# Kernel optimization log

Measured on AMD Instinct MI355X. Metric: run time of the kernel, lower is better.

Reference implementation:

```python
import jax, jax.numpy as jnp
import numpy as np

B, NSEQ, SEQ_PER = 2, 4, 256
S = NSEQ * SEQ_PER            # total sequence (stocks interleaved along seq dim)
D, H, HD = 1024, 16, 64       # d_model, nhead, head_dim
HD2, HD4 = HD // 2, HD // 4
DFF = 4096
LAMBDA_INIT = 0.2             # lambda_init_fn(0) = 0.8 - 0.6*exp(0)
SCALING = 1.0 / float(np.sqrt(HD2))
EPS_DEF = float(np.finfo(np.float32).eps)   # torch RMSNorm default eps (eps=None)
EPS_ATTN = 1e-5


def _rms(x, w, eps):
    return x * jax.lax.rsqrt(jnp.mean(x * x, axis=-1, keepdims=True) + eps) * w


def _rope(x, fc):
    # x: (B, T, NSEQ, 2H, HD2); fc: (T, HD4, 2) holding (cos, sin)
    xr = x.reshape(x.shape[:-1] + (HD4, 2))
    c = fc[None, :, None, None, :, 0]
    s = fc[None, :, None, None, :, 1]
    x0, x1 = xr[..., 0], xr[..., 1]
    return jnp.stack([x0 * c - x1 * s, x0 * s + x1 * c], axis=-1).reshape(x.shape)


def setup_inputs():
    key = jax.random.key(0)
    ks = jax.random.split(key, 16)
    def w(i, shape, std=0.02):
        return jax.random.normal(ks[i], shape, jnp.float32) * std
    # true RoPE table for seq_per_stock-1 positions
    t = jnp.arange(SEQ_PER - 1, dtype=jnp.float32)[:, None]
    inv = 1.0 / (10000.0 ** (jnp.arange(HD4, dtype=jnp.float32) / HD4))
    ang = t * inv[None, :]
    return {
        "x": jax.random.normal(ks[0], (B, S, D), jnp.float32),
        "freqs_cis": jnp.stack([jnp.cos(ang), jnp.sin(ang)], axis=-1),
        "w_norm1": jnp.ones((D,), jnp.float32),
        "w_norm2": jnp.ones((D,), jnp.float32),
        "Wq": w(1, (H * HD, D)), "bq": jnp.zeros((H * HD,), jnp.float32),
        "Wk": w(2, (H * HD, D)), "bk": jnp.zeros((H * HD,), jnp.float32),
        "Wv": w(3, (H * HD, D)), "bv": jnp.zeros((H * HD,), jnp.float32),
        "Wo": w(4, (D, H * HD)), "bo": jnp.zeros((D,), jnp.float32),
        "lq1": w(5, (HD2,), 0.1), "lk1": w(6, (HD2,), 0.1),
        "lq2": w(7, (HD2,), 0.1), "lk2": w(8, (HD2,), 0.1),
        "w_attn_norm": jnp.ones((HD,), jnp.float32),
        "Wg": w(9, (2 * DFF, D)), "bg": jnp.zeros((2 * DFF,), jnp.float32),
        "Wout": w(10, (D, DFF)), "bout": jnp.zeros((D,), jnp.float32),
    }


def reference(x, freqs_cis, w_norm1, w_norm2, Wq, bq, Wk, bk, Wv, bv, Wo, bo,
              lq1, lk1, lq2, lk2, w_attn_norm, Wg, bg, Wout, bout):
    Bz, Sz, _ = x.shape
    h = _rms(x, w_norm1, EPS_DEF)
    q = (h @ Wq.T + bq).reshape(Bz, SEQ_PER, NSEQ, 2 * H, HD2)
    k = (h @ Wk.T + bk).reshape(Bz, SEQ_PER, NSEQ, 2 * H, HD2)
    v = (h @ Wv.T + bv).reshape(Bz, Sz, H, HD).transpose(0, 2, 1, 3)   # (B,H,S,HD), interleaved order
    # RoPE on all but the first per-stock timestep; same freqs for every stock
    q = jnp.concatenate([q[:, :1], _rope(q[:, 1:], freqs_cis)], axis=1)
    k = jnp.concatenate([k[:, :1], _rope(k[:, 1:], freqs_cis)], axis=1)
    # reorder q/k to stock-major flat sequence (torch permute(0,4,1,2,3)+reshape)
    q = q.transpose(0, 2, 1, 3, 4).reshape(Bz, Sz, 2 * H, HD2).transpose(0, 2, 1, 3)
    k = k.transpose(0, 2, 1, 3, 4).reshape(Bz, Sz, 2 * H, HD2).transpose(0, 2, 1, 3)
    scores = jnp.einsum('bhqd,bhkd->bhqk', q, k) * SCALING              # (B,2H,S,S)
    causal = jnp.triu(jnp.ones((SEQ_PER, SEQ_PER), bool), 1)
    mask = jnp.tile(causal, (NSEQ, NSEQ))   # block-tiled causal, as torch .repeat
    att = jnp.sign(scores) * jax.nn.softmax(
        jnp.where(mask, -1e30, jnp.abs(scores)), axis=-1)
    lam = jnp.exp(jnp.sum(lk1 * lq1)) - jnp.exp(jnp.sum(lk2 * lq2)) + LAMBDA_INIT
    att = att.reshape(Bz, H, 2, Sz, Sz)
    a1, a2 = att[:, :, 0], att[:, :, 1]
    G = jnp.mean(a1, axis=-2, keepdims=True)          # mean over queries, broadcast back
    a = jnp.where(mask, 0.0, a1 - lam * a2 + lam * G)
    ao = jnp.einsum('bhqk,bhkd->bhqd', a, v)          # v kept in interleaved order (faithful to source)
    ao = _rms(ao, w_attn_norm, EPS_ATTN)
    ao = ao.reshape(Bz, Sz, H * HD)  # flat reinterpret (B,H,S,HD)->(B,S,H*HD), matches torch reshape chain
    x = x + ao @ Wo.T + bo
    h2 = _rms(x, w_norm2, EPS_DEF)
    u, vg = jnp.split(h2 @ Wg.T + bg, 2, axis=-1)
    return x + (u * jax.nn.silu(vg)) @ Wout.T + bout
```

## Files before the change

### kernel.cpp

```cpp
#include <hip/hip_runtime.h>

#define LAMBDA_INIT 0.2f
#define SCALING 0.17677669529663687f
#define EPS_DEF 1.1920928955078125e-07f
#define EPS_ATTN 1e-5f

typedef unsigned short us4 __attribute__((ext_vector_type(4)));
typedef unsigned short us8v __attribute__((ext_vector_type(8)));
typedef float f32x4 __attribute__((ext_vector_type(4)));
typedef float f32x2 __attribute__((ext_vector_type(2)));
typedef __bf16 bf16x8 __attribute__((ext_vector_type(8)));

#define MFMA16(a, b, c) __builtin_amdgcn_mfma_f32_16x16x32_bf16((a), (b), (c), 0, 0, 0)

__device__ __forceinline__ float bf2f(unsigned short u) {
    unsigned int x = ((unsigned int)u) << 16;
    return __builtin_bit_cast(float, x);
}
__device__ __forceinline__ unsigned short f2bf(float f) {
    unsigned int x = __builtin_bit_cast(unsigned int, f);
    x += 0x7fffu + ((x >> 16) & 1u);
    return (unsigned short)(x >> 16);
}
__device__ __forceinline__ void split8(f32x4 a, f32x4 b, us8v& hi, us8v& lo) {
#pragma unroll
    for (int u = 0; u < 4; u++) {
        unsigned short h = f2bf(a[u]);
        hi[u] = h; lo[u] = f2bf(a[u] - bf2f(h));
        unsigned short h2 = f2bf(b[u]);
        hi[4 + u] = h2; lo[4 + u] = f2bf(b[u] - bf2f(h2));
    }
}
__device__ __forceinline__ bf16x8 ldb(const unsigned short* p) {
    return __builtin_bit_cast(bf16x8, *(const us8v*)p);
}

__device__ __forceinline__ float wave_sum(float v) {
#pragma unroll
    for (int o = 32; o > 0; o >>= 1) v += __shfl_down(v, o);
    return v;
}
__device__ __forceinline__ float block_sum(float v, float* red4) {
    int wv = threadIdx.x >> 6;
    float w = wave_sum(v);
    __syncthreads();
    if ((threadIdx.x & 63) == 0) red4[wv] = w;
    __syncthreads();
    return red4[0] + red4[1] + red4[2] + red4[3];
}

__global__ __launch_bounds__(256) void prep(float* __restrict__ G, float* __restrict__ lamp,
                                            const float* lq1, const float* lk1,
                                            const float* lq2, const float* lk2) {
    int i = (blockIdx.x * 256 + threadIdx.x) * 4;
    G[i] = 0.f; G[i + 1] = 0.f; G[i + 2] = 0.f; G[i + 3] = 0.f;
    if (blockIdx.x == 0 && threadIdx.x == 0) {
        float a = 0.f, c = 0.f;
        for (int d = 0; d < 32; d++) {
            a += lq1[d] * lk1[d];
            c += lq2[d] * lk2[d];
        }
        *lamp = expf(a) - expf(c) + LAMBDA_INIT;
    }
}

__global__ __launch_bounds__(256) void cvt_bf16(const float* __restrict__ s,
                                                unsigned short* __restrict__ d, int n4) {
    int i = blockIdx.x * 256 + threadIdx.x;
    if (i >= n4) return;
    f32x4 v = ((const f32x4*)s)[i];
    us4 o;
#pragma unroll
    for (int u = 0; u < 4; u++) o[u] = f2bf(v[u]);
    ((us4*)d)[i] = o;
}

__global__ __launch_bounds__(256) void cvt_split(const float* __restrict__ s,
                                                 unsigned short* __restrict__ hi,
                                                 unsigned short* __restrict__ lo, int n4) {
    int i = blockIdx.x * 256 + threadIdx.x;
    if (i >= n4) return;
    f32x4 v = ((const f32x4*)s)[i];
    us4 h, l;
#pragma unroll
    for (int u = 0; u < 4; u++) {
        h[u] = f2bf(v[u]);
        l[u] = f2bf(v[u] - bf2f(h[u]));
    }
    ((us4*)hi)[i] = h;
    ((us4*)lo)[i] = l;
}

template <int OUTBF>
__global__ __launch_bounds__(256) void rms_kernel(const float* __restrict__ x,
                                                  const float* __restrict__ w,
                                                  void* __restrict__ out, float eps) {
    int row = blockIdx.x;
    int tid = threadIdx.x;
    size_t base = (size_t)row * 1024 + tid * 4;
    f32x4 v = *(const f32x4*)(x + base);
    float ss = v[0]*v[0] + v[1]*v[1] + v[2]*v[2] + v[3]*v[3];
    __shared__ float red4[4];
    float tot = block_sum(ss, red4);
    float r = rsqrtf(tot * (1.0f / 1024.f) + eps);
    f32x4 wv = *(const f32x4*)(w + tid * 4);
    if (OUTBF) {
        us4 o;
#pragma unroll
        for (int i = 0; i < 4; i++) o[i] = f2bf(v[i] * r * wv[i]);
        *(us4*)((unsigned short*)out + base) = o;
    } else {
        f32x4 o;
#pragma unroll
        for (int i = 0; i < 4; i++) o[i] = v[i] * r * wv[i];
        *(f32x4*)((float*)out + base) = o;
    }
}

__global__ __launch_bounds__(256) void rms_split(const float* __restrict__ x,
                                                 const float* __restrict__ w,
                                                 unsigned short* __restrict__ hh,
                                                 unsigned short* __restrict__ hl, float eps) {
    int row = blockIdx.x;
    int tid = threadIdx.x;
    size_t base = (size_t)row * 1024 + tid * 4;
    f32x4 v = *(const f32x4*)(x + base);
    float ss = v[0]*v[0] + v[1]*v[1] + v[2]*v[2] + v[3]*v[3];
    __shared__ float red4[4];
    float tot = block_sum(ss, red4);
    float r = rsqrtf(tot * (1.0f / 1024.f) + eps);
    f32x4 wv = *(const f32x4*)(w + tid * 4);
    us4 oh, ol;
#pragma unroll
    for (int i = 0; i < 4; i++) {
        float val = v[i] * r * wv[i];
        oh[i] = f2bf(val);
        ol[i] = f2bf(val - bf2f(oh[i]));
    }
    *(us4*)(hh + base) = oh;
    *(us4*)(hl + base) = ol;
}

__global__ __launch_bounds__(256) void gemm_qkv_ps(
        const unsigned short* __restrict__ AH, const unsigned short* __restrict__ AL,
        const unsigned short* __restrict__ WqH, const unsigned short* __restrict__ WqL,
        const unsigned short* __restrict__ WkH, const unsigned short* __restrict__ WkL,
        const unsigned short* __restrict__ WvH, const unsigned short* __restrict__ WvL,
        const float* __restrict__ bq, const float* __restrict__ bk, const float* __restrict__ bv,
        float* __restrict__ Yq, float* __restrict__ Yk, float* __restrict__ Yv) {
    const int z = blockIdx.z;
    const unsigned short* BH = (z == 0) ? WqH : (z == 1) ? WkH : WvH;
    const unsigned short* BL = (z == 0) ? WqL : (z == 1) ? WkL : WvL;
    const float* bias = (z == 0) ? bq : (z == 1) ? bk : bv;
    float* out        = (z == 0) ? Yq : (z == 1) ? Yk : Yv;
    const int K = 1024, N = 1024;
    __shared__ __align__(16) unsigned short Ah[64][72];
    __shared__ __align__(16) unsigned short Al[64][72];
    __shared__ __align__(16) unsigned short Bh[64][72];
    __shared__ __align__(16) unsigned short Bl[64][72];
    const int t = threadIdx.x;
    const int bm = blockIdx.x, bn = blockIdx.y;
    const int lane = t & 63, w = t >> 6;
    const int wr = w >> 1, wc = w & 1;
    const int l15 = lane & 15, lg = lane >> 4;
    const int sr = t >> 2, sc = (t & 3) * 16;

    const unsigned short* AgH = AH + (size_t)(bm * 64 + sr) * K + sc;
    const unsigned short* AgL = AL + (size_t)(bm * 64 + sr) * K + sc;
    const unsigned short* BgH = BH + (size_t)(bn * 64 + sr) * K + sc;
    const unsigned short* BgL = BL + (size_t)(bn * 64 + sr) * K + sc;

    f32x4 acc[2][2] = {};

    for (int k0 = 0; k0 < K; k0 += 64) {
        us8v ah0 = *(const us8v*)(AgH + k0), ah1 = *(const us8v*)(AgH + k0 + 8);
        us8v al0 = *(const us8v*)(AgL + k0), al1 = *(const us8v*)(AgL + k0 + 8);
        us8v bh0 = *(const us8v*)(BgH + k0), bh1 = *(const us8v*)(BgH + k0 + 8);
        us8v bl0 = *(const us8v*)(BgL + k0), bl1 = *(const us8v*)(BgL + k0 + 8);
        __syncthreads();
        *(us8v*)&Ah[sr][sc] = ah0; *(us8v*)&Ah[sr][sc + 8] = ah1;
        *(us8v*)&Al[sr][sc] = al0; *(us8v*)&Al[sr][sc + 8] = al1;
        *(us8v*)&Bh[sr][sc] = bh0; *(us8v*)&Bh[sr][sc + 8] = bh1;
        *(us8v*)&Bl[sr][sc] = bl0; *(us8v*)&Bl[sr][sc + 8] = bl1;
        __syncthreads();
#pragma unroll
        for (int kk = 0; kk < 2; kk++) {
            bf16x8 afh[2], afl[2], bfh[2], bfl[2];
#pragma unroll
            for (int mi = 0; mi < 2; mi++) {
                afh[mi] = ldb(&Ah[wr * 32 + mi * 16 + l15][kk * 32 + lg * 8]);
                afl[mi] = ldb(&Al[wr * 32 + mi * 16 + l15][kk * 32 + lg * 8]);
            }
#pragma unroll
            for (int ni = 0; ni < 2; ni++) {
                bfh[ni] = ldb(&Bh[wc * 32 + ni * 16 + l15][kk * 32 + lg * 8]);
                bfl[ni] = ldb(&Bl[wc * 32 + ni * 16 + l15][kk * 32 + lg * 8]);
            }
#pragma unroll
            for (int mi = 0; mi < 2; mi++)
#pragma unroll
                for (int ni = 0; ni < 2; ni++) {
                    acc[mi][ni] = MFMA16(afl[mi], bfh[ni], acc[mi][ni]);
                    acc[mi][ni] = MFMA16(afh[mi], bfl[ni], acc[mi][ni]);
                    acc[mi][ni] = MFMA16(afh[mi], bfh[ni], acc[mi][ni]);
                }
        }
    }

    const int rbase = bm * 64 + wr * 32 + (lg << 2);
    const int cbase = bn * 64 + wc * 32 + l15;
#pragma unroll
    for (int mi = 0; mi < 2; mi++) {
#pragma unroll
        for (int ni = 0; ni < 2; ni++) {
            int col = cbase + ni * 16;
            float bb = bias[col];
#pragma unroll
            for (int r = 0; r < 4; r++) {
                int row = rbase + mi * 16 + r;
                out[(size_t)row * N + col] = acc[mi][ni][r] + bb;
            }
        }
    }
}

__global__ __launch_bounds__(256) void gemm_mfma_wb(const unsigned short* __restrict__ A,
                                                    const unsigned short* __restrict__ Bt,
                                                    const float* __restrict__ bias,
                                                    const float* __restrict__ res,
                                                    float* __restrict__ out,
                                                    int M, int N, int K) {
    __shared__ __align__(16) unsigned short As[64][72];
    __shared__ __align__(16) unsigned short Bs[64][72];
    const int t = threadIdx.x;
    const int bm = blockIdx.x, bn = blockIdx.y;
    const int lane = t & 63, w = t >> 6;
    const int wr = w >> 1, wc = w & 1;
    const int l15 = lane & 15, lg = lane >> 4;
    const int sr = t >> 2, sc = (t & 3) * 16;

    const unsigned short* Ag = A + (size_t)(bm * 64 + sr) * K + sc;
    const unsigned short* Bg = Bt + (size_t)(bn * 64 + sr) * K + sc;

    f32x4 acc[2][2] = {};

    for (int k0 = 0; k0 < K; k0 += 64) {
        us8v a0 = *(const us8v*)(Ag + k0);
        us8v a1 = *(const us8v*)(Ag + k0 + 8);
        us8v b0 = *(const us8v*)(Bg + k0);
        us8v b1 = *(const us8v*)(Bg + k0 + 8);
        __syncthreads();
        *(us8v*)&As[sr][sc]     = a0;
        *(us8v*)&As[sr][sc + 8] = a1;
        *(us8v*)&Bs[sr][sc]     = b0;
        *(us8v*)&Bs[sr][sc + 8] = b1;
        __syncthreads();
#pragma unroll
        for (int kk = 0; kk < 2; kk++) {
            bf16x8 af[2], bf[2];
#pragma unroll
            for (int mi = 0; mi < 2; mi++)
                af[mi] = ldb(&As[wr * 32 + mi * 16 + l15][kk * 32 + lg * 8]);
#pragma unroll
            for (int ni = 0; ni < 2; ni++)
                bf[ni] = ldb(&Bs[wc * 32 + ni * 16 + l15][kk * 32 + lg * 8]);
#pragma unroll
            for (int mi = 0; mi < 2; mi++)
#pragma unroll
                for (int ni = 0; ni < 2; ni++)
                    acc[mi][ni] = MFMA16(af[mi], bf[ni], acc[mi][ni]);
        }
    }

    const int rbase = bm * 64 + wr * 32 + (lg << 2);
    const int cbase = bn * 64 + wc * 32 + l15;
#pragma unroll
    for (int mi = 0; mi < 2; mi++) {
#pragma unroll
        for (int ni = 0; ni < 2; ni++) {
            int col = cbase + ni * 16;
            float bb = bias[col];
#pragma unroll
            for (int r = 0; r < 4; r++) {
                int row = rbase + mi * 16 + r;
                size_t oi = (size_t)row * N + col;
                out[oi] = acc[mi][ni][r] + bb + res[oi];
            }
        }
    }
}

__global__ __launch_bounds__(256) void gemm_gate_mfma(const unsigned short* __restrict__ A,
                                                      const float* __restrict__ Wg,
                                                      const float* __restrict__ bg,
                                                      unsigned short* __restrict__ mlp) {
    __shared__ __align__(16) unsigned short As[128][72];
    __shared__ __align__(16) unsigned short BsU[64][72];
    __shared__ __align__(16) unsigned short BsV[64][72];
    const int t = threadIdx.x;
    const int bm = blockIdx.x, bn = blockIdx.y;
    const int lane = t & 63, w = t >> 6;
    const int wr = w >> 1, wc = w & 1;
    const int l15 = lane & 15, lg = lane >> 4;
    const int sr = t >> 2, sc = (t & 3) * 16;

    const unsigned short* Ag  = A + (size_t)(bm * 128 + sr) * 1024 + sc;
    const unsigned short* Ag2 = Ag + (size_t)64 * 1024;
    const float* BgU = Wg + (size_t)(bn * 64 + sr) * 1024 + sc;
    const float* BgV = Wg + (size_t)(4096 + bn * 64 + sr) * 1024 + sc;

    f32x4 accU[4][2] = {};
    f32x4 accV[4][2] = {};

    for (int k0 = 0; k0 < 1024; k0 += 64) {
        us8v a0 = *(const us8v*)(Ag + k0);
        us8v a1 = *(const us8v*)(Ag + k0 + 8);
        us8v a2 = *(const us8v*)(Ag2 + k0);
        us8v a3 = *(const us8v*)(Ag2 + k0 + 8);
        f32x4 u0 = *(const f32x4*)(BgU + k0);
        f32x4 u1 = *(const f32x4*)(BgU + k0 + 4);
        f32x4 u2 = *(const f32x4*)(BgU + k0 + 8);
        f32x4 u3 = *(const f32x4*)(BgU + k0 + 12);
        f32x4 v0 = *(const f32x4*)(BgV + k0);
        f32x4 v1 = *(const f32x4*)(BgV + k0 + 4);
        f32x4 v2 = *(const f32x4*)(BgV + k0 + 8);
        f32x4 v3 = *(const f32x4*)(BgV + k0 + 12);
        us8v uw0, uw1, vw0, vw1;
#pragma unroll
        for (int u = 0; u < 4; u++) {
            uw0[u] = f2bf(u0[u]); uw0[4 + u] = f2bf(u1[u]);
            uw1[u] = f2bf(u2[u]); uw1[4 + u] = f2bf(u3[u]);
            vw0[u] = f2bf(v0[u]); vw0[4 + u] = f2bf(v1[u]);
            vw1[u] = f2bf(v2[u]); vw1[4 + u] = f2bf(v3[u]);
        }
        __syncthreads();
        *(us8v*)&As[sr][sc]          = a0;
        *(us8v*)&As[sr][sc + 8]      = a1;
        *(us8v*)&As[sr + 64][sc]     = a2;
        *(us8v*)&As[sr + 64][sc + 8] = a3;
        *(us8v*)&BsU[sr][sc]         = uw0;
        *(us8v*)&BsU[sr][sc + 8]     = uw1;
        *(us8v*)&BsV[sr][sc]         = vw0;
        *(us8v*)&BsV[sr][sc + 8]     = vw1;
        __syncthreads();
#pragma unroll
        for (int kk = 0; kk < 2; kk++) {
            bf16x8 af[4], bu[2], bv2[2];
#pragma unroll
            for (int mi = 0; mi < 4; mi++)
                af[mi] = ldb(&As[wr * 64 + mi * 16 + l15][kk * 32 + lg * 8]);
#pragma unroll
            for (int ni = 0; ni < 2; ni++) {
                bu[ni]  = ldb(&BsU[wc * 32 + ni * 16 + l15][kk * 32 + lg * 8]);
                bv2[ni] = ldb(&BsV[wc * 32 + ni * 16 + l15][kk * 32 + lg * 8]);
            }
#pragma unroll
            for (int mi = 0; mi < 4; mi++)
#pragma unroll
                for (int ni = 0; ni < 2; ni++) {
                    accU[mi][ni] = MFMA16(af[mi], bu[ni], accU[mi][ni]);
                    accV[mi][ni] = MFMA16(af[mi], bv2[ni], accV[mi][ni]);
                }
        }
    }

    const int rbase = bm * 128 + wr * 64 + (lg << 2);
    const int cbase = bn * 64 + wc * 32 + l15;
#pragma unroll
    for (int mi = 0; mi < 4; mi++) {
#pragma unroll
        for (int ni = 0; ni < 2; ni++) {
            int col = cbase + ni * 16;
            float bu_ = bg[col], bv_ = bg[4096 + col];
#pragma unroll
            for (int r = 0; r < 4; r++) {
                int row = rbase + mi * 16 + r;
                float u = accU[mi][ni][r] + bu_;
                float v = accV[mi][ni][r] + bv_;
                float s = v / (1.f + __expf(-v));
                mlp[(size_t)row * 4096 + col] = f2bf(u * s);
            }
        }
    }
}

__global__ __launch_bounds__(256) void rope_inplace(float* __restrict__ Y,
                                                    const float* __restrict__ fc) {
    int t = blockIdx.x;
    int s = t & 1023;
    int p = s >> 2;
    if (p == 0) return;
    int c0 = threadIdx.x * 4;
    float* y = Y + (size_t)t * 1024 + c0;
    int d4 = (c0 & 31) >> 1;
    f32x4 f = *(const f32x4*)(fc + ((size_t)(p - 1) * 16 + d4) * 2);
    float v0 = y[0], v1 = y[1], v2 = y[2], v3 = y[3];
    y[0] = v0 * f[0] - v1 * f[1];
    y[1] = v0 * f[1] + v1 * f[0];
    y[2] = v2 * f[2] - v3 * f[3];
    y[3] = v2 * f[3] + v3 * f[2];
}

__global__ __launch_bounds__(256) void rope_split_k(const float* __restrict__ Yk,
                                                    const float* __restrict__ fc,
                                                    unsigned short* __restrict__ KhG,
                                                    unsigned short* __restrict__ KlG) {
    int t = blockIdx.x;
    int s = t & 1023;
    int p = s >> 2;
    int c0 = threadIdx.x * 4;
    const float* y = Yk + (size_t)t * 1024 + c0;
    float v0 = y[0], v1 = y[1], v2 = y[2], v3 = y[3];
    if (p > 0) {
        int d4 = (c0 & 31) >> 1;
        f32x4 f = *(const f32x4*)(fc + ((size_t)(p - 1) * 16 + d4) * 2);
        float w0 = v0 * f[0] - v1 * f[1];
        float w1 = v0 * f[1] + v1 * f[0];
        float w2 = v2 * f[2] - v3 * f[3];
        float w3 = v2 * f[3] + v3 * f[2];
        v0 = w0; v1 = w1; v2 = w2; v3 = w3;
    }
    us4 hi, lo;
    hi[0] = f2bf(v0); lo[0] = f2bf(v0 - bf2f(hi[0]));
    hi[1] = f2bf(v1); lo[1] = f2bf(v1 - bf2f(hi[1]));
    hi[2] = f2bf(v2); lo[2] = f2bf(v2 - bf2f(hi[2]));
    hi[3] = f2bf(v3); lo[3] = f2bf(v3 - bf2f(hi[3]));
    *(us4*)(KhG + (size_t)t * 1024 + c0) = hi;
    *(us4*)(KlG + (size_t)t * 1024 + c0) = lo;
}

__global__ __launch_bounds__(256) void v_split_t(const float* __restrict__ Yv,
                                                 unsigned short* __restrict__ VtH,
                                                 unsigned short* __restrict__ VtL) {
    const int jc = blockIdx.x, h = blockIdx.y, b = blockIdx.z;
    __shared__ float tile[64][65];
    const int t = threadIdx.x;
    {
        const int jr = t >> 2, dc = (t & 3) * 16;
        const float* src = Yv + ((size_t)(b * 1024 + jc * 64 + jr) << 10) + h * 64 + dc;
        *(f32x4*)&tile[jr][dc]      = *(const f32x4*)src;
        *(f32x4*)&tile[jr][dc + 4]  = *(const f32x4*)(src + 4);
        *(f32x4*)&tile[jr][dc + 8]  = *(const f32x4*)(src + 8);
        *(f32x4*)&tile[jr][dc + 12] = *(const f32x4*)(src + 12);
    }
    __syncthreads();
    const int d = t >> 2, js = (t & 3) * 16;
    us8v h0, h1, l0, l1;
#pragma unroll
    for (int n = 0; n < 16; n++) {
        float val = tile[js + n][d];
        unsigned short hh = f2bf(val);
        unsigned short ll = f2bf(val - bf2f(hh));
        if (n < 8) { h0[n] = hh; l0[n] = ll; }
        else       { h1[n - 8] = hh; l1[n - 8] = ll; }
    }
    size_t ob = (((size_t)(b * 16 + h) * 64 + d) << 10) + jc * 64 + js;
    *(us8v*)(VtH + ob) = h0; *(us8v*)(VtH + ob + 8) = h1;
    *(us8v*)(VtL + ob) = l0; *(us8v*)(VtL + ob + 8) = l1;
}

__global__ __launch_bounds__(256) void pass_1(const float* __restrict__ Yq,
                                              const unsigned short* __restrict__ KhG,
                                              const unsigned short* __restrict__ KlG,
                                              const unsigned short* __restrict__ VtH,
                                              const unsigned short* __restrict__ VtL,
                                              const float* __restrict__ lamp,
                                              float* __restrict__ G,
                                              float* __restrict__ AOp) {
    const int blk = blockIdx.x;
    const int p  = blk >> 5;
    const int h  = blk & 15;
    const int b  = (blk >> 4) & 1;
    const int t = threadIdx.x;
    const int lane = t & 63, w = t >> 6;
    const int l15 = lane & 15, lg = lane >> 4;

    __shared__ __align__(16) unsigned short Kh[64][72];
    __shared__ __align__(16) unsigned short Kl[64][72];
    __shared__ __align__(16) unsigned short Vth[64][72];
    __shared__ __align__(16) unsigned short Vtl[64][72];
    __shared__ __align__(16) unsigned short Wh[64][72];
    __shared__ __align__(16) unsigned short Wl[64][72];
    __shared__ float Gacc[1024];

    for (int i = t; i < 1024; i += 256) Gacc[i] = 0.f;

    const int srow = t >> 2, ssub = t & 3;
    const int ptk = 4 * (srow & 15) + (srow >> 4);
    const unsigned short* KhB = KhG + ((size_t)(b * 1024) << 10) + h * 64;
    const unsigned short* KlB = KlG + ((size_t)(b * 1024) << 10) + h * 64;
    const unsigned short* VhB = VtH + (((size_t)(b * 16 + h) * 64 + srow) << 10) + ssub * 256;
    const unsigned short* VlB = VtL + (((size_t)(b * 16 + h) * 64 + srow) << 10) + ssub * 256;
    const float lam = *lamp;
    const int dq0 = w * 16 + (lg << 2);

    for (int qq = 0; qq < 2; qq++) {
        const int qc = qq ? p : (15 - p);

        us8v qh[2], ql[2];
        {
            const float* qp = Yq + ((size_t)(b * 1024 + qc * 64 + w * 16 + l15) << 10)
                              + h * 64 + lg * 8;
#pragma unroll
            for (int H = 0; H < 2; H++)
                split8(*(const f32x4*)(qp + H * 32), *(const f32x4*)(qp + H * 32 + 4), qh[H], ql[H]);
        }

        float z1r[4] = {0.f, 0.f, 0.f, 0.f};
        float z2r[4] = {0.f, 0.f, 0.f, 0.f};

        for (int kc = 0; kc <= qc; kc++) {
            __syncthreads();
            {
                const unsigned short* kh = KhB + ((size_t)(kc * 64 + ptk) << 10) + ssub * 16;
                const unsigned short* kl = KlB + ((size_t)(kc * 64 + ptk) << 10) + ssub * 16;
                *(us8v*)&Kh[srow][ssub * 16]     = *(const us8v*)kh;
                *(us8v*)&Kh[srow][ssub * 16 + 8] = *(const us8v*)(kh + 8);
                *(us8v*)&Kl[srow][ssub * 16]     = *(const us8v*)kl;
                *(us8v*)&Kl[srow][ssub * 16 + 8] = *(const us8v*)(kl + 8);
            }
            __syncthreads();
            const int kpos = kc * 16 + l15;
#pragma unroll
            for (int kf = 0; kf < 4; kf++) {
                const int krow = kf * 16 + l15;
                const int kcol = lg * 8;
                bf16x8 b1h = ldb(&Kh[krow][kcol]),      b1l = ldb(&Kl[krow][kcol]);
                bf16x8 b2h = ldb(&Kh[krow][32 + kcol]), b2l = ldb(&Kl[krow][32 + kcol]);
                f32x4 s1 = {}, s2 = {};
                s1 = MFMA16(__builtin_bit_cast(bf16x8, ql[0]), b1h, s1);
                s1 = MFMA16(__builtin_bit_cast(bf16x8, qh[0]), b1l, s1);
                s1 = MFMA16(__builtin_bit_cast(bf16x8, qh[0]), b1h, s1);
                s2 = MFMA16(__builtin_bit_cast(bf16x8, ql[1]), b2h, s2);
                s2 = MFMA16(__builtin_bit_cast(bf16x8, qh[1]), b2l, s2);
                s2 = MFMA16(__builtin_bit_cast(bf16x8, qh[1]), b2h, s2);
#pragma unroll
                for (int r = 0; r < 4; r++) {
                    int pq = (qc * 64 + dq0 + r) >> 2;
                    if (kpos <= pq) {
                        z1r[r] += __expf(fabsf(s1[r] * SCALING));
                        z2r[r] += __expf(fabsf(s2[r] * SCALING));
                    }
                }
            }
        }
#pragma unroll
        for (int r = 0; r < 4; r++) {
            float a = z1r[r];
            a += __shfl_xor(a, 1); a += __shfl_xor(a, 2);
            a += __shfl_xor(a, 4); a += __shfl_xor(a, 8);
            z1r[r] = 1.f / fmaxf(a, 1e-20f);
            float c = z2r[r];
            c += __shfl_xor(c, 1); c += __shfl_xor(c, 2);
            c += __shfl_xor(c, 4); c += __shfl_xor(c, 8);
            z2r[r] = 1.f / fmaxf(c, 1e-20f);
        }

        f32x4 ao[4] = {};

        for (int kc = 0; kc <= qc; kc++) {
            __syncthreads();
            {
                const unsigned short* kh = KhB + ((size_t)(kc * 64 + ptk) << 10) + ssub * 16;
                const unsigned short* kl = KlB + ((size_t)(kc * 64 + ptk) << 10) + ssub * 16;
                *(us8v*)&Kh[srow][ssub * 16]     = *(const us8v*)kh;
                *(us8v*)&Kh[srow][ssub * 16 + 8] = *(const us8v*)(kh + 8);
                *(us8v*)&Kl[srow][ssub * 16]     = *(const us8v*)kl;
                *(us8v*)&Kl[srow][ssub * 16 + 8] = *(const us8v*)(kl + 8);
                const unsigned short* vh = VhB + kc * 16;
                const unsigned short* vl = VlB + kc * 16;
                *(us8v*)&Vth[srow][ssub * 16]     = *(const us8v*)vh;
                *(us8v*)&Vth[srow][ssub * 16 + 8] = *(const us8v*)(vh + 8);
                *(us8v*)&Vtl[srow][ssub * 16]     = *(const us8v*)vl;
                *(us8v*)&Vtl[srow][ssub * 16 + 8] = *(const us8v*)(vl + 8);
            }
            __syncthreads();
            const int kpos = kc * 16 + l15;
#pragma unroll
            for (int kf = 0; kf < 4; kf++) {
                const int krow = kf * 16 + l15;
                const int kcol = lg * 8;
                bf16x8 b1h = ldb(&Kh[krow][kcol]),      b1l = ldb(&Kl[krow][kcol]);
                bf16x8 b2h = ldb(&Kh[krow][32 + kcol]), b2l = ldb(&Kl[krow][32 + kcol]);
                f32x4 s1 = {}, s2 = {};
                s1 = MFMA16(__builtin_bit_cast(bf16x8, ql[0]), b1h, s1);
                s1 = MFMA16(__builtin_bit_cast(bf16x8, qh[0]), b1l, s1);
                s1 = MFMA16(__builtin_bit_cast(bf16x8, qh[0]), b1h, s1);
                s2 = MFMA16(__builtin_bit_cast(bf16x8, ql[1]), b2h, s2);
                s2 = MFMA16(__builtin_bit_cast(bf16x8, qh[1]), b2l, s2);
                s2 = MFMA16(__builtin_bit_cast(bf16x8, qh[1]), b2h, s2);
                const int kli = kf * 16 + l15;
                float colsum = 0.f;
#pragma unroll
                for (int r = 0; r < 4; r++) {
                    int pq = (qc * 64 + dq0 + r) >> 2;
                    float wv = 0.f, a1 = 0.f;
                    if (kpos <= pq) {
                        float t1 = s1[r] * SCALING, t2 = s2[r] * SCALING;
                        float sg1 = (t1 > 0.f) ? 1.f : ((t1 < 0.f) ? -1.f : 0.f);
                        float sg2 = (t2 > 0.f) ? 1.f : ((t2 < 0.f) ? -1.f : 0.f);
                        a1 = sg1 * __expf(fabsf(t1)) * z1r[r];
                        wv = a1 - lam * (sg2 * __expf(fabsf(t2)) * z2r[r]);
                    }
                    colsum += a1;
                    unsigned short hh = f2bf(wv);
                    Wh[dq0 + r][kli] = hh;
                    Wl[dq0 + r][kli] = f2bf(wv - bf2f(hh));
                }
                colsum += __shfl_xor(colsum, 16);
                colsum += __shfl_xor(colsum, 32);
                if (lane < 16) atomicAdd(&Gacc[kf * 256 + kc * 16 + lane], colsum);
            }
            __syncthreads();
#pragma unroll
            for (int kh2 = 0; kh2 < 2; kh2++) {
                bf16x8 wah = ldb(&Wh[w * 16 + l15][kh2 * 32 + lg * 8]);
                bf16x8 wal = ldb(&Wl[w * 16 + l15][kh2 * 32 + lg * 8]);
#pragma unroll
                for (int df = 0; df < 4; df++) {
                    bf16x8 vbh = ldb(&Vth[df * 16 + l15][kh2 * 32 + lg * 8]);
                    bf16x8 vbl = ldb(&Vtl[df * 16 + l15][kh2 * 32 + lg * 8]);
                    ao[df] = MFMA16(wah, vbl, ao[df]);
                    ao[df] = MFMA16(wal, vbh, ao[df]);
                    ao[df] = MFMA16(wah, vbh, ao[df]);
                }
            }
        }

#pragma unroll
        for (int df = 0; df < 4; df++) {
#pragma unroll
            for (int r = 0; r < 4; r++) {
                int tq = qc * 64 + dq0 + r;
                int qrow = ((tq & 3) << 8) + (tq >> 2);
                AOp[((((size_t)(b * 16 + h)) << 10) + qrow) * 64 + df * 16 + l15] = ao[df][r];
            }
        }
    }

    __syncthreads();
    float* Gb = G + ((size_t)(b * 16 + h) << 10);
    const int limp = (16 - p) << 4;
    for (int idx = t; idx < 1024; idx += 256) {
        if ((idx & 255) < limp) atomicAdd(&Gb[idx], Gacc[idx]);
    }
}

__global__ __launch_bounds__(256) void pass_2a(const float* __restrict__ G,
                                               const float* __restrict__ Yv,
                                               float* __restrict__ GVpre) {
    const int h = blockIdx.x, b = blockIdx.y;
    const int t = threadIdx.x;
    __shared__ float Gl[1024];
    __shared__ float S[256][64];
    __shared__ float segsum[4][64];
    for (int i = t; i < 1024; i += 256) Gl[i] = G[((size_t)(b * 16 + h) << 10) + i];
    __syncthreads();
    const int d = t & 63, pg = t >> 6;
    const float* Yvb = Yv + ((size_t)b << 20) + h * 64 + d;
    for (int p0 = 0; p0 < 64; p0++) {
        int pos = pg * 64 + p0;
        float s = 0.f;
#pragma unroll
        for (int sq = 0; sq < 4; sq++) {
            int j = (sq << 8) + pos;
            s += Gl[j] * Yvb[(size_t)j << 10];
        }
        S[pos][d] = s;
    }
    __syncthreads();
    float acc = 0.f;
    for (int p0 = 0; p0 < 64; p0++) {
        int pos = pg * 64 + p0;
        acc += S[pos][d];
        S[pos][d] = acc;
    }
    segsum[pg][d] = acc;
    __syncthreads();
    float off = 0.f;
    for (int g = 0; g < pg; g++) off += segsum[g][d];
    float* gv = GVpre + (((size_t)(b * 16 + h)) << 14) + d;
    for (int p0 = 0; p0 < 64; p0++) {
        int pos = pg * 64 + p0;
        gv[pos << 6] = S[pos][d] + off;
    }
}

__global__ __launch_bounds__(256) void pass_2b(const float* __restrict__ AOp,
                                               const float* __restrict__ GVpre,
                                               const float* __restrict__ lamp,
                                               const float* __restrict__ wan,
                                               unsigned short* __restrict__ aoS) {
    const int qg = blockIdx.x;
    const int h = blockIdx.y, b = blockIdx.z;
    const int t = threadIdx.x;
    const int d = t & 63, rg = t >> 6;
    const float lamg = (*lamp) * (1.f / 1024.f);
    const float wv = wan[d];
    const float* aob = AOp + ((((size_t)(b * 16 + h)) << 10) + (qg << 8)) * 64 + d;
    const float* gvb = GVpre + (((size_t)(b * 16 + h)) << 14) + d;
    unsigned short* ob = aoS + ((size_t)b << 20) + ((size_t)h << 16) + ((size_t)(qg << 8) << 6) + d;
    for (int p0 = 0; p0 < 64; p0++) {
        int pq = p0 * 4 + rg;
        float ao = aob[(size_t)pq << 6] + lamg * gvb[(size_t)pq << 6];
        float ss = ao * ao;
#pragma unroll
        for (int o = 1; o < 64; o <<= 1) ss += __shfl_xor(ss, o);
        float rr_ = rsqrtf(ss * (1.f / 64.f) + EPS_ATTN);
        ob[(size_t)pq << 6] = f2bf(ao * rr_ * wv);
    }
}

extern "C" void kernel_launch(void* const* d_in, const int* in_sizes, int n_in,
                              void* d_out, int out_size, void* d_ws, size_t ws_size,
                              hipStream_t stream) {
    const float* x    = (const float*)d_in[0];
    const float* fc   = (const float*)d_in[1];
    const float* w1   = (const float*)d_in[2];
    const float* w2   = (const float*)d_in[3];
    const float* Wq   = (const float*)d_in[4];
    const float* bq   = (const float*)d_in[5];
    const float* Wk   = (const float*)d_in[6];
    const float* bk   = (const float*)d_in[7];
    const float* Wv   = (const float*)d_in[8];
    const float* bv   = (const float*)d_in[9];
    const float* Wo   = (const float*)d_in[10];
    const float* bo   = (const float*)d_in[11];
    const float* lq1  = (const float*)d_in[12];
    const float* lk1  = (const float*)d_in[13];
    const float* lq2  = (const float*)d_in[14];
    const float* lk2  = (const float*)d_in[15];
    const float* wan  = (const float*)d_in[16];
    const float* Wg   = (const float*)d_in[17];
    const float* bg   = (const float*)d_in[18];
    const float* Wout = (const float*)d_in[19];
    const float* bout = (const float*)d_in[20];

    char* ws = (char*)d_ws;
    const size_t MB = 1024 * 1024;
    float* G    = (float*)(ws);
    float* lam  = (float*)(ws + 256 * 1024);
    unsigned short* hH = (unsigned short*)(ws + 1 * MB);
    unsigned short* hL = (unsigned short*)(ws + 5 * MB);
    float* Yq   = (float*)(ws + 9 * MB);
    float* Yk   = (float*)(ws + 17 * MB);
    float* Yv   = (float*)(ws + 25 * MB);
    unsigned short* WqH = (unsigned short*)(ws + 33 * MB);
    unsigned short* WqL = (unsigned short*)(ws + 35 * MB);
    unsigned short* WkH = (unsigned short*)(ws + 37 * MB);
    unsigned short* WkL = (unsigned short*)(ws + 39 * MB);
    unsigned short* WvH = (unsigned short*)(ws + 41 * MB);
    unsigned short* WvL = (unsigned short*)(ws + 43 * MB);
    unsigned short* WoutB = (unsigned short*)(ws + 45 * MB);
    float* AOp  = (float*)(ws + 33 * MB);
    float* GVpre= (float*)(ws + 41 * MB);
    unsigned short* WoB = (unsigned short*)(ws + 43 * MB);
    unsigned short* KhG = (unsigned short*)(ws + 1 * MB);
    unsigned short* KlG = (unsigned short*)(ws + 5 * MB);
    unsigned short* VtH = (unsigned short*)(ws + 17 * MB);
    unsigned short* VtL = (unsigned short*)(ws + 21 * MB);
    unsigned short* aoS = (unsigned short*)(ws + 1 * MB);
    float* X1           = (float*)(ws + 9 * MB);
    unsigned short* h2b = (unsigned short*)(ws + 5 * MB);
    unsigned short* mlp = (unsigned short*)(ws + 17 * MB);

    prep<<<32, 256, 0, stream>>>(G, lam, lq1, lk1, lq2, lk2);
    cvt_bf16<<<4096, 256, 0, stream>>>(Wout, WoutB, 1048576);
    rms_split<<<2048, 256, 0, stream>>>(x, w1, hH, hL, EPS_DEF);
    cvt_split<<<1024, 256, 0, stream>>>(Wq, WqH, WqL, 262144);
    cvt_split<<<1024, 256, 0, stream>>>(Wk, WkH, WkL, 262144);
    cvt_split<<<1024, 256, 0, stream>>>(Wv, WvH, WvL, 262144);
    gemm_qkv_ps<<<dim3(32, 16, 3), 256, 0, stream>>>(hH, hL, WqH, WqL, WkH, WkL, WvH, WvL,
                                                     bq, bk, bv, Yq, Yk, Yv);
    cvt_bf16<<<1024, 256, 0, stream>>>(Wo, WoB, 262144);
    rope_inplace<<<2048, 256, 0, stream>>>(Yq, fc);
    rope_split_k<<<2048, 256, 0, stream>>>(Yk, fc, KhG, KlG);
    v_split_t<<<dim3(16, 16, 2), 256, 0, stream>>>(Yv, VtH, VtL);
    pass_1<<<256, 256, 0, stream>>>(Yq, KhG, KlG, VtH, VtL, lam, G, AOp);
    pass_2a<<<dim3(16, 2), 256, 0, stream>>>(G, Yv, GVpre);
    pass_2b<<<dim3(4, 16, 2), 256, 0, stream>>>(AOp, GVpre, lam, wan, aoS);
    dim3 gmf(32, 16);
    gemm_mfma_wb<<<gmf, 256, 0, stream>>>(aoS, WoB, bo, x, X1, 2048, 1024, 1024);
    rms_kernel<1><<<2048, 256, 0, stream>>>(X1, w2, h2b, EPS_DEF);
    gemm_gate_mfma<<<dim3(16, 64), 256, 0, stream>>>(h2b, Wg, bg, mlp);
    gemm_mfma_wb<<<gmf, 256, 0, stream>>>(mlp, WoutB, bout, X1, (float*)d_out, 2048, 1024, 4096);
}
```

Before: 464.4 us.

## Prefetch next tiles into registers in GEMMs and split attention pass per query chunk

Both MFMA GEMM kernels now load the next K tile from global memory into registers right after the shared-memory store, so the load latency overlaps with the MFMA work on the current tile. The attention pass_1 kernel no longer has each block handle a pair of query chunks (qc and 15-qc). It launches 512 blocks, one per query chunk, with the largest chunks scheduled first. Its K/V loops use the same register prefetch. This trades the earlier load-balanced pairing for more parallelism and latency hiding, at the cost of more registers, uneven block lengths and more atomics into G.

New measurement: 439.2 us. -5.4%, faster.

```diff
diff --git a/kernel.cpp b/kernel.cpp
--- a/kernel.cpp
+++ b/kernel.cpp
@@ -172,17 +172,25 @@
 
     f32x4 acc[2][2] = {};
 
+    us8v ah0 = *(const us8v*)AgH, ah1 = *(const us8v*)(AgH + 8);
+    us8v al0 = *(const us8v*)AgL, al1 = *(const us8v*)(AgL + 8);
+    us8v bh0 = *(const us8v*)BgH, bh1 = *(const us8v*)(BgH + 8);
+    us8v bl0 = *(const us8v*)BgL, bl1 = *(const us8v*)(BgL + 8);
+
     for (int k0 = 0; k0 < K; k0 += 64) {
-        us8v ah0 = *(const us8v*)(AgH + k0), ah1 = *(const us8v*)(AgH + k0 + 8);
-        us8v al0 = *(const us8v*)(AgL + k0), al1 = *(const us8v*)(AgL + k0 + 8);
-        us8v bh0 = *(const us8v*)(BgH + k0), bh1 = *(const us8v*)(BgH + k0 + 8);
-        us8v bl0 = *(const us8v*)(BgL + k0), bl1 = *(const us8v*)(BgL + k0 + 8);
         __syncthreads();
         *(us8v*)&Ah[sr][sc] = ah0; *(us8v*)&Ah[sr][sc + 8] = ah1;
         *(us8v*)&Al[sr][sc] = al0; *(us8v*)&Al[sr][sc + 8] = al1;
         *(us8v*)&Bh[sr][sc] = bh0; *(us8v*)&Bh[sr][sc + 8] = bh1;
         *(us8v*)&Bl[sr][sc] = bl0; *(us8v*)&Bl[sr][sc + 8] = bl1;
         __syncthreads();
+        if (k0 + 64 < K) {
+            const int kn = k0 + 64;
+            ah0 = *(const us8v*)(AgH + kn); ah1 = *(const us8v*)(AgH + kn + 8);
+            al0 = *(const us8v*)(AgL + kn); al1 = *(const us8v*)(AgL + kn + 8);
+            bh0 = *(const us8v*)(BgH + kn); bh1 = *(const us8v*)(BgH + kn + 8);
+            bl0 = *(const us8v*)(BgL + kn); bl1 = *(const us8v*)(BgL + kn + 8);
+        }
 #pragma unroll
         for (int kk = 0; kk < 2; kk++) {
             bf16x8 afh[2], afl[2], bfh[2], bfl[2];
@@ -244,17 +252,21 @@
 
     f32x4 acc[2][2] = {};
 
+    us8v a0 = *(const us8v*)Ag, a1 = *(const us8v*)(Ag + 8);
+    us8v b0 = *(const us8v*)Bg, b1 = *(const us8v*)(Bg + 8);
+
     for (int k0 = 0; k0 < K; k0 += 64) {
-        us8v a0 = *(const us8v*)(Ag + k0);
-        us8v a1 = *(const us8v*)(Ag + k0 + 8);
-        us8v b0 = *(const us8v*)(Bg + k0);
-        us8v b1 = *(const us8v*)(Bg + k0 + 8);
         __syncthreads();
         *(us8v*)&As[sr][sc]     = a0;
         *(us8v*)&As[sr][sc + 8] = a1;
         *(us8v*)&Bs[sr][sc]     = b0;
         *(us8v*)&Bs[sr][sc + 8] = b1;
         __syncthreads();
+        if (k0 + 64 < K) {
+            const int kn = k0 + 64;
+            a0 = *(const us8v*)(Ag + kn); a1 = *(const us8v*)(Ag + kn + 8);
+            b0 = *(const us8v*)(Bg + kn); b1 = *(const us8v*)(Bg + kn + 8);
+        }
 #pragma unroll
         for (int kk = 0; kk < 2; kk++) {
             bf16x8 af[2], bf[2];
@@ -468,7 +480,7 @@
                                               float* __restrict__ G,
                                               float* __restrict__ AOp) {
     const int blk = blockIdx.x;
-    const int p  = blk >> 5;
+    const int qc = 15 - (blk >> 5);
     const int h  = blk & 15;
     const int b  = (blk >> 4) & 1;
     const int t = threadIdx.x;
@@ -485,6 +497,16 @@
 
     for (int i = t; i < 1024; i += 256) Gacc[i] = 0.f;
 
+    us8v qh[2], ql[2];
+    {
+        const float* qp = Yq + ((size_t)(b * 1024 + qc * 64 + w * 16 + l15) << 10)
+                          + h * 64 + lg * 8;
+#pragma unroll
+        for (int H = 0; H < 2; H++)
+            split8(*(const f32x4*)(qp + H * 32), *(const f32x4*)(qp + H * 32 + 4), qh[H], ql[H]);
+    }
+    const int dq0 = w * 16 + (lg << 2);
+
     const int srow = t >> 2, ssub = t & 3;
     const int ptk = 4 * (srow & 15) + (srow >> 4);
     const unsigned short* KhB = KhG + ((size_t)(b * 1024) << 10) + h * 64;
@@ -492,155 +514,163 @@
     const unsigned short* VhB = VtH + (((size_t)(b * 16 + h) * 64 + srow) << 10) + ssub * 256;
     const unsigned short* VlB = VtL + (((size_t)(b * 16 + h) * 64 + srow) << 10) + ssub * 256;
     const float lam = *lamp;
-    const int dq0 = w * 16 + (lg << 2);
-
-    for (int qq = 0; qq < 2; qq++) {
-        const int qc = qq ? p : (15 - p);
-
-        us8v qh[2], ql[2];
-        {
-            const float* qp = Yq + ((size_t)(b * 1024 + qc * 64 + w * 16 + l15) << 10)
-                              + h * 64 + lg * 8;
-#pragma unroll
-            for (int H = 0; H < 2; H++)
-                split8(*(const f32x4*)(qp + H * 32), *(const f32x4*)(qp + H * 32 + 4), qh[H], ql[H]);
-        }
-
-        float z1r[4] = {0.f, 0.f, 0.f, 0.f};
-        float z2r[4] = {0.f, 0.f, 0.f, 0.f};
-
-        for (int kc = 0; kc <= qc; kc++) {
-            __syncthreads();
-            {
-                const unsigned short* kh = KhB + ((size_t)(kc * 64 + ptk) << 10) + ssub * 16;
-                const unsigned short* kl = KlB + ((size_t)(kc * 64 + ptk) << 10) + ssub * 16;
-                *(us8v*)&Kh[srow][ssub * 16]     = *(const us8v*)kh;
-                *(us8v*)&Kh[srow][ssub * 16 + 8] = *(const us8v*)(kh + 8);
-                *(us8v*)&Kl[srow][ssub * 16]     = *(const us8v*)kl;
-                *(us8v*)&Kl[srow][ssub * 16 + 8] = *(const us8v*)(kl + 8);
-            }
-            __syncthreads();
-            const int kpos = kc * 16 + l15;
-#pragma unroll
-            for (int kf = 0; kf < 4; kf++) {
-                const int krow = kf * 16 + l15;
-                const int kcol = lg * 8;
-                bf16x8 b1h = ldb(&Kh[krow][kcol]),      b1l = ldb(&Kl[krow][kcol]);
-                bf16x8 b2h = ldb(&Kh[krow][32 + kcol]), b2l = ldb(&Kl[krow][32 + kcol]);
-                f32x4 s1 = {}, s2 = {};
-                s1 = MFMA16(__builtin_bit_cast(bf16x8, ql[0]), b1h, s1);
-                s1 = MFMA16(__builtin_bit_cast(bf16x8, qh[0]), b1l, s1);
-                s1 = MFMA16(__builtin_bit_cast(bf16x8, qh[0]), b1h, s1);
-                s2 = MFMA16(__builtin_bit_cast(bf16x8, ql[1]), b2h, s2);
-                s2 = MFMA16(__builtin_bit_cast(bf16x8, qh[1]), b2l, s2);
-                s2 = MFMA16(__builtin_bit_cast(bf16x8, qh[1]), b2h, s2);
-#pragma unroll
-                for (int r = 0; r < 4; r++) {
-                    int pq = (qc * 64 + dq0 + r) >> 2;
-                    if (kpos <= pq) {
-                        z1r[r] += __expf(fabsf(s1[r] * SCALING));
-                        z2r[r] += __expf(fabsf(s2[r] * SCALING));
-                    }
+
+    float z1r[4] = {0.f, 0.f, 0.f, 0.f};
+    float z2r[4] = {0.f, 0.f, 0.f, 0.f};
+
+    us8v rkh0, rkh1, rkl0, rkl1;
+    {
+        const unsigned short* kh = KhB + ((size_t)ptk << 10) + ssub * 16;
+        const unsigned short* kl = KlB + ((size_t)ptk << 10) + ssub * 16;
+        rkh0 = *(const us8v*)kh; rkh1 = *(const us8v*)(kh + 8);
+        rkl0 = *(const us8v*)kl; rkl1 = *(const us8v*)(kl + 8);
+    }
+    for (int kc = 0; kc <= qc; kc++) {
+        __syncthreads();
+        *(us8v*)&Kh[srow][ssub * 16]     = rkh0;
+        *(us8v*)&Kh[srow][ssub * 16 + 8] = rkh1;
+        *(us8v*)&Kl[srow][ssub * 16]     = rkl0;
+        *(us8v*)&Kl[srow][ssub * 16 + 8] = rkl1;
+        __syncthreads();
+        if (kc < qc) {
+            const unsigned short* kh = KhB + ((size_t)((kc + 1) * 64 + ptk) << 10) + ssub * 16;
+            const unsigned short* kl = KlB + ((size_t)((kc + 1) * 64 + ptk) << 10) + ssub * 16;
+            rkh0 = *(const us8v*)kh; rkh1 = *(const us8v*)(kh + 8);
+            rkl0 = *(const us8v*)kl; rkl1 = *(const us8v*)(kl + 8);
+        }
+        const int kpos = kc * 16 + l15;
+#pragma unroll
+        for (int kf = 0; kf < 4; kf++) {
+            const int krow = kf * 16 + l15;
+            const int kcol = lg * 8;
+            bf16x8 b1h = ldb(&Kh[krow][kcol]),      b1l = ldb(&Kl[krow][kcol]);
+            bf16x8 b2h = ldb(&Kh[krow][32 + kcol]), b2l = ldb(&Kl[krow][32 + kcol]);
+            f32x4 s1 = {}, s2 = {};
+            s1 = MFMA16(__builtin_bit_cast(bf16x8, ql[0]), b1h, s1);
+            s1 = MFMA16(__builtin_bit_cast(bf16x8, qh[0]), b1l, s1);
+            s1 = MFMA16(__builtin_bit_cast(bf16x8, qh[0]), b1h, s1);
+            s2 = MFMA16(__builtin_bit_cast(bf16x8, ql[1]), b2h, s2);
+            s2 = MFMA16(__builtin_bit_cast(bf16x8, qh[1]), b2l, s2);
+            s2 = MFMA16(__builtin_bit_cast(bf16x8, qh[1]), b2h, s2);
+#pragma unroll
+            for (int r = 0; r < 4; r++) {
+                int pq = (qc * 64 + dq0 + r) >> 2;
+                if (kpos <= pq) {
+                    z1r[r] += __expf(fabsf(s1[r] * SCALING));
+                    z2r[r] += __expf(fabsf(s2[r] * SCALING));
                 }
             }
         }
+    }
+#pragma unroll
+    for (int r = 0; r < 4; r++) {
+        float a = z1r[r];
+        a += __shfl_xor(a, 1); a += __shfl_xor(a, 2);
+        a += __shfl_xor(a, 4); a += __shfl_xor(a, 8);
+        z1r[r] = 1.f / fmaxf(a, 1e-20f);
+        float c = z2r[r];
+        c += __shfl_xor(c, 1); c += __shfl_xor(c, 2);
+        c += __shfl_xor(c, 4); c += __shfl_xor(c, 8);
+        z2r[r] = 1.f / fmaxf(c, 1e-20f);
+    }
+
+    f32x4 ao[4] = {};
+
+    us8v rvh0, rvh1, rvl0, rvl1;
+    {
+        const unsigned short* kh = KhB + ((size_t)ptk << 10) + ssub * 16;
+        const unsigned short* kl = KlB + ((size_t)ptk << 10) + ssub * 16;
+        rkh0 = *(const us8v*)kh; rkh1 = *(const us8v*)(kh + 8);
+        rkl0 = *(const us8v*)kl; rkl1 = *(const us8v*)(kl + 8);
+        rvh0 = *(const us8v*)VhB; rvh1 = *(const us8v*)(VhB + 8);
+        rvl0 = *(const us8v*)VlB; rvl1 = *(const us8v*)(VlB + 8);
+    }
+    for (int kc = 0; kc <= qc; kc++) {
+        __syncthreads();
+        *(us8v*)&Kh[srow][ssub * 16]      = rkh0;
+        *(us8v*)&Kh[srow][ssub * 16 + 8]  = rkh1;
+        *(us8v*)&Kl[srow][ssub * 16]      = rkl0;
+        *(us8v*)&Kl[srow][ssub * 16 + 8]  = rkl1;
+        *(us8v*)&Vth[srow][ssub * 16]     = rvh0;
+        *(us8v*)&Vth[srow][ssub * 16 + 8] = rvh1;
+        *(us8v*)&Vtl[srow][ssub * 16]     = rvl0;
+        *(us8v*)&Vtl[srow][ssub * 16 + 8] = rvl1;
+        __syncthreads();
+        if (kc < qc) {
+            const unsigned short* kh = KhB + ((size_t)((kc + 1) * 64 + ptk) << 10) + ssub * 16;
+            const unsigned short* kl = KlB + ((size_t)((kc + 1) * 64 + ptk) << 10) + ssub * 16;
+            rkh0 = *(const us8v*)kh; rkh1 = *(const us8v*)(kh + 8);
+            rkl0 = *(const us8v*)kl; rkl1 = *(const us8v*)(kl + 8);
+            const unsigned short* vh = VhB + (kc + 1) * 16;
+            const unsigned short* vl = VlB + (kc + 1) * 16;
+            rvh0 = *(const us8v*)vh; rvh1 = *(const us8v*)(vh + 8);
+            rvl0 = *(const us8v*)vl; rvl1 = *(const us8v*)(vl + 8);
+        }
+        const int kpos = kc * 16 + l15;
+#pragma unroll
+        for (int kf = 0; kf < 4; kf++) {
+            const int krow = kf * 16 + l15;
+            const int kcol = lg * 8;
+            bf16x8 b1h = ldb(&Kh[krow][kcol]),      b1l = ldb(&Kl[krow][kcol]);
+            bf16x8 b2h = ldb(&Kh[krow][32 + kcol]), b2l = ldb(&Kl[krow][32 + kcol]);
+            f32x4 s1 = {}, s2 = {};
+            s1 = MFMA16(__builtin_bit_cast(bf16x8, ql[0]), b1h, s1);
+            s1 = MFMA16(__builtin_bit_cast(bf16x8, qh[0]), b1l, s1);
+            s1 = MFMA16(__builtin_bit_cast(bf16x8, qh[0]), b1h, s1);
+            s2 = MFMA16(__builtin_bit_cast(bf16x8, ql[1]), b2h, s2);
+            s2 = MFMA16(__builtin_bit_cast(bf16x8, qh[1]), b2l, s2);
+            s2 = MFMA16(__builtin_bit_cast(bf16x8, qh[1]), b2h, s2);
+            const int kli = kf * 16 + l15;
+            float colsum = 0.f;
+#pragma unroll
+            for (int r = 0; r < 4; r++) {
+                int pq = (qc * 64 + dq0 + r) >> 2;
+                float wv = 0.f, a1 = 0.f;
+                if (kpos <= pq) {
+                    float t1 = s1[r] * SCALING, t2 = s2[r] * SCALING;
+                    float sg1 = (t1 > 0.f) ? 1.f : ((t1 < 0.f) ? -1.f : 0.f);
+                    float sg2 = (t2 > 0.f) ? 1.f : ((t2 < 0.f) ? -1.f : 0.f);
+                    a1 = sg1 * __expf(fabsf(t1)) * z1r[r];
+                    wv = a1 - lam * (sg2 * __expf(fabsf(t2)) * z2r[r]);
+                }
+                colsum += a1;
+                unsigned short hh = f2bf(wv);
+                Wh[dq0 + r][kli] = hh;
+                Wl[dq0 + r][kli] = f2bf(wv - bf2f(hh));
+            }
+            colsum += __shfl_xor(colsum, 16);
+            colsum += __shfl_xor(colsum, 32);
+            if (lane < 16) atomicAdd(&Gacc[kf * 256 + kc * 16 + lane], colsum);
+        }
+        __syncthreads();
+#pragma unroll
+        for (int kh2 = 0; kh2 < 2; kh2++) {
+            bf16x8 wah = ldb(&Wh[w * 16 + l15][kh2 * 32 + lg * 8]);
+            bf16x8 wal = ldb(&Wl[w * 16 + l15][kh2 * 32 + lg * 8]);
+#pragma unroll
+            for (int df = 0; df < 4; df++) {
+                bf16x8 vbh = ldb(&Vth[df * 16 + l15][kh2 * 32 + lg * 8]);
+                bf16x8 vbl = ldb(&Vtl[df * 16 + l15][kh2 * 32 + lg * 8]);
+                ao[df] = MFMA16(wah, vbl, ao[df]);
+                ao[df] = MFMA16(wal, vbh, ao[df]);
+                ao[df] = MFMA16(wah, vbh, ao[df]);
+            }
+        }
+    }
+
+#pragma unroll
+    for (int df = 0; df < 4; df++) {
 #pragma unroll
         for (int r = 0; r < 4; r++) {
-            float a = z1r[r];
-            a += __shfl_xor(a, 1); a += __shfl_xor(a, 2);
-            a += __shfl_xor(a, 4); a += __shfl_xor(a, 8);
-            z1r[r] = 1.f / fmaxf(a, 1e-20f);
-            float c = z2r[r];
-            c += __shfl_xor(c, 1); c += __shfl_xor(c, 2);
-            c += __shfl_xor(c, 4); c += __shfl_xor(c, 8);
-            z2r[r] = 1.f / fmaxf(c, 1e-20f);
-        }
-
-        f32x4 ao[4] = {};
-
-        for (int kc = 0; kc <= qc; kc++) {
-            __syncthreads();
-            {
-                const unsigned short* kh = KhB + ((size_t)(kc * 64 + ptk) << 10) + ssub * 16;
-                const unsigned short* kl = KlB + ((size_t)(kc * 64 + ptk) << 10) + ssub * 16;
-                *(us8v*)&Kh[srow][ssub * 16]     = *(const us8v*)kh;
-                *(us8v*)&Kh[srow][ssub * 16 + 8] = *(const us8v*)(kh + 8);
-                *(us8v*)&Kl[srow][ssub * 16]     = *(const us8v*)kl;
-                *(us8v*)&Kl[srow][ssub * 16 + 8] = *(const us8v*)(kl + 8);
-                const unsigned short* vh = VhB + kc * 16;
-                const unsigned short* vl = VlB + kc * 16;
-                *(us8v*)&Vth[srow][ssub * 16]     = *(const us8v*)vh;
-                *(us8v*)&Vth[srow][ssub * 16 + 8] = *(const us8v*)(vh + 8);
-                *(us8v*)&Vtl[srow][ssub * 16]     = *(const us8v*)vl;
-                *(us8v*)&Vtl[srow][ssub * 16 + 8] = *(const us8v*)(vl + 8);
-            }
-            __syncthreads();
-            const int kpos = kc * 16 + l15;
-#pragma unroll
-            for (int kf = 0; kf < 4; kf++) {
-                const int krow = kf * 16 + l15;
-                const int kcol = lg * 8;
-                bf16x8 b1h = ldb(&Kh[krow][kcol]),      b1l = ldb(&Kl[krow][kcol]);
-                bf16x8 b2h = ldb(&Kh[krow][32 + kcol]), b2l = ldb(&Kl[krow][32 + kcol]);
-                f32x4 s1 = {}, s2 = {};
-                s1 = MFMA16(__builtin_bit_cast(bf16x8, ql[0]), b1h, s1);
-                s1 = MFMA16(__builtin_bit_cast(bf16x8, qh[0]), b1l, s1);
-                s1 = MFMA16(__builtin_bit_cast(bf16x8, qh[0]), b1h, s1);
-                s2 = MFMA16(__builtin_bit_cast(bf16x8, ql[1]), b2h, s2);
-                s2 = MFMA16(__builtin_bit_cast(bf16x8, qh[1]), b2l, s2);
-                s2 = MFMA16(__builtin_bit_cast(bf16x8, qh[1]), b2h, s2);
-                const int kli = kf * 16 + l15;
-                float colsum = 0.f;
-#pragma unroll
-                for (int r = 0; r < 4; r++) {
-                    int pq = (qc * 64 + dq0 + r) >> 2;
-                    float wv = 0.f, a1 = 0.f;
-                    if (kpos <= pq) {
-                        float t1 = s1[r] * SCALING, t2 = s2[r] * SCALING;
-                        float sg1 = (t1 > 0.f) ? 1.f : ((t1 < 0.f) ? -1.f : 0.f);
-                        float sg2 = (t2 > 0.f) ? 1.f : ((t2 < 0.f) ? -1.f : 0.f);
-                        a1 = sg1 * __expf(fabsf(t1)) * z1r[r];
-                        wv = a1 - lam * (sg2 * __expf(fabsf(t2)) * z2r[r]);
-                    }
-                    colsum += a1;
-                    unsigned short hh = f2bf(wv);
-                    Wh[dq0 + r][kli] = hh;
-                    Wl[dq0 + r][kli] = f2bf(wv - bf2f(hh));
-                }
-                colsum += __shfl_xor(colsum, 16);
-                colsum += __shfl_xor(colsum, 32);
-                if (lane < 16) atomicAdd(&Gacc[kf * 256 + kc * 16 + lane], colsum);
-            }
-            __syncthreads();
-#pragma unroll
-            for (int kh2 = 0; kh2 < 2; kh2++) {
-                bf16x8 wah = ldb(&Wh[w * 16 + l15][kh2 * 32 + lg * 8]);
-                bf16x8 wal = ldb(&Wl[w * 16 + l15][kh2 * 32 + lg * 8]);
-#pragma unroll
-                for (int df = 0; df < 4; df++) {
-                    bf16x8 vbh = ldb(&Vth[df * 16 + l15][kh2 * 32 + lg * 8]);
-                    bf16x8 vbl = ldb(&Vtl[df * 16 + l15][kh2 * 32 + lg * 8]);
-                    ao[df] = MFMA16(wah, vbl, ao[df]);
-                    ao[df] = MFMA16(wal, vbh, ao[df]);
-                    ao[df] = MFMA16(wah, vbh, ao[df]);
-                }
-            }
-        }
-
-#pragma unroll
-        for (int df = 0; df < 4; df++) {
-#pragma unroll
-            for (int r = 0; r < 4; r++) {
-                int tq = qc * 64 + dq0 + r;
-                int qrow = ((tq & 3) << 8) + (tq >> 2);
-                AOp[((((size_t)(b * 16 + h)) << 10) + qrow) * 64 + df * 16 + l15] = ao[df][r];
-            }
+            int tq = qc * 64 + dq0 + r;
+            int qrow = ((tq & 3) << 8) + (tq >> 2);
+            AOp[((((size_t)(b * 16 + h)) << 10) + qrow) * 64 + df * 16 + l15] = ao[df][r];
         }
     }
 
     __syncthreads();
     float* Gb = G + ((size_t)(b * 16 + h) << 10);
-    const int limp = (16 - p) << 4;
+    const int limp = (qc + 1) << 4;
     for (int idx = t; idx < 1024; idx += 256) {
         if ((idx & 255) < limp) atomicAdd(&Gb[idx], Gacc[idx]);
     }
@@ -776,7 +806,7 @@
     rope_inplace<<<2048, 256, 0, stream>>>(Yq, fc);
     rope_split_k<<<2048, 256, 0, stream>>>(Yk, fc, KhG, KlG);
     v_split_t<<<dim3(16, 16, 2), 256, 0, stream>>>(Yv, VtH, VtL);
-    pass_1<<<256, 256, 0, stream>>>(Yq, KhG, KlG, VtH, VtL, lam, G, AOp);
+    pass_1<<<512, 256, 0, stream>>>(Yq, KhG, KlG, VtH, VtL, lam, G, AOp);
     pass_2a<<<dim3(16, 2), 256, 0, stream>>>(G, Yv, GVpre);
     pass_2b<<<dim3(4, 16, 2), 256, 0, stream>>>(AOp, GVpre, lam, wan, aoS);
     dim3 gmf(32, 16);
```
